# Kernel optimization log

Hardware: AMD Instinct MI355X
Metric: run time of the kernel (lower is better)

The kernel has to match this reference:

```python
import jax, jax.numpy as jnp
import numpy as np

DIMS = 256
HID = 512


def setup_inputs() -> dict:
    key = jax.random.key(0)
    ks = jax.random.split(key, 12)
    s = 0.1
    inp = {
        'x': jax.random.normal(ks[0], (64, 2048, DIMS), dtype=jnp.float32),
        'h': jnp.zeros((64, HID), jnp.float32),
        'c': jnp.zeros((64, HID), jnp.float32),
        'W_j': jax.random.normal(ks[1], (DIMS, HID), jnp.float32) * s,
        'W_i': jax.random.normal(ks[2], (DIMS, HID), jnp.float32) * s,
        'W_f': jax.random.normal(ks[3], (DIMS, HID), jnp.float32) * s,
        'W_o': jax.random.normal(ks[4], (DIMS, HID), jnp.float32) * s,
        'U_j': jax.random.normal(ks[5], (HID, HID), jnp.float32) * s,
        'U_i': jax.random.normal(ks[6], (HID, HID), jnp.float32) * s,
        'U_f': jax.random.normal(ks[7], (HID, HID), jnp.float32) * s,
        'U_o': jax.random.normal(ks[8], (HID, HID), jnp.float32) * s,
        'b_j': jnp.zeros((1, HID), jnp.float32),
        'b_i': jnp.zeros((1, HID), jnp.float32),
        'b_f': jnp.zeros((1, HID), jnp.float32),
        'b_o': jnp.zeros((1, HID), jnp.float32),
        'W_y': jax.random.normal(ks[9], (HID, DIMS), jnp.float32) * s,
        'b_y': jnp.zeros((1, DIMS), jnp.float32),
    }
    return inp


def reference(x, h, c, W_j, W_i, W_f, W_o, U_j, U_i, U_f, U_o,
              b_j, b_i, b_f, b_o, W_y, b_y):
    # Precompute input projections for all timesteps: [B,T,H] -> [T,B,H]
    xj = jnp.einsum('btd,dh->tbh', x, W_j) + b_j
    xi = jnp.einsum('btd,dh->tbh', x, W_i) + b_i
    xf = jnp.einsum('btd,dh->tbh', x, W_f) + b_f
    xo = jnp.einsum('btd,dh->tbh', x, W_o) + b_o

    def step(carry, xs):
        h, c = carry
        pj, pi, pf, po = xs
        # NOTE: module defaults -> j,i,o sigmoid; f tanh; cell activation tanh
        j = jax.nn.sigmoid(pj + h @ U_j)
        i = jax.nn.sigmoid(pi + h @ U_i)
        f = jnp.tanh(pf + h @ U_f)
        o = jax.nn.sigmoid(po + h @ U_o)
        c = f * c + i * j
        h = o * jnp.tanh(c)
        return (h, c), h

    (h_last, c_last), hs = jax.lax.scan(step, (h, c), (xj, xi, xf, xo))
    # hs: [T,B,H] -> y_hat: [B,T,dims]
    y_hat = jnp.einsum('tbh,hd->btd', hs, W_y) + b_y
    return y_hat, h_last, c_last
```

## Files before the change

kernel.cpp:

```cpp
#include <hip/hip_runtime.h>


typedef __attribute__((ext_vector_type(8))) short bf16x8;
typedef __attribute__((ext_vector_type(4))) float f32x4;

#define T_STEPS 2048
#define DIMS 256
#define HID 512

#define NPACK_U  1048576
#define NPACK_WX 524288
#define NPACK_WY 131072

#define OFF_UHI   0u
#define OFF_ULO   2097152u
#define OFF_WXHI  4194304u
#define OFF_WXLO  5242880u
#define OFF_WYHI  6291456u
#define OFF_WYLO  6553600u
#define OFF_HBUF  6815744u
#define OFF_FLAGS 7077888u

__device__ __forceinline__ unsigned short f2bf(float f) {
    unsigned u = __float_as_uint(f);
    return (unsigned short)((u + 0x7fffu + ((u >> 16) & 1u)) >> 16);
}
__device__ __forceinline__ float bf2f(unsigned short h) {
    return __uint_as_float((unsigned)h << 16);
}
__device__ __forceinline__ void split2(float f, unsigned short& hi, unsigned short& lo) {
    hi = f2bf(f);
    lo = f2bf(f - bf2f(hi));
}
__device__ __forceinline__ float sigf(float x) { return 1.0f / (1.0f + __expf(-x)); }
__device__ __forceinline__ float tanhfast(float x) { return 2.0f * sigf(2.0f * x) - 1.0f; }

__global__ void lstm_prep(const float* __restrict__ Uj, const float* __restrict__ Ui,
                          const float* __restrict__ Uf, const float* __restrict__ Uo,
                          const float* __restrict__ Wj, const float* __restrict__ Wi,
                          const float* __restrict__ Wf, const float* __restrict__ Wo,
                          const float* __restrict__ Wy,
                          unsigned short* __restrict__ Uph, unsigned short* __restrict__ Upl,
                          unsigned short* __restrict__ Wxh, unsigned short* __restrict__ Wxl,
                          unsigned short* __restrict__ Wyh, unsigned short* __restrict__ Wyl,
                          unsigned* __restrict__ flags) {
    int idx = blockIdx.x * 256 + threadIdx.x;
    if (idx < NPACK_U) {
        int j = idx & 7, l = (idx >> 3) & 63, ks = (idx >> 9) & 15, nt = (idx >> 13) & 7, s = (idx >> 16) & 15;
        int gate = nt >> 1;
        int hu = s * 32 + (nt & 1) * 16 + (l & 15);
        int k = ks * 32 + ((l >> 4) << 3) + j;
        const float* U = (gate == 0) ? Uj : (gate == 1) ? Ui : (gate == 2) ? Uf : Uo;
        unsigned short hi, lo; split2(U[k * HID + hu], hi, lo);
        Uph[idx] = hi; Upl[idx] = lo;
    } else if (idx < NPACK_U + NPACK_WX) {
        int i2 = idx - NPACK_U;
        int j = i2 & 7, l = (i2 >> 3) & 63, ks = (i2 >> 9) & 7, nt = (i2 >> 12) & 7, s = (i2 >> 15) & 15;
        int gate = nt >> 1;
        int hu = s * 32 + (nt & 1) * 16 + (l & 15);
        int k = ks * 32 + ((l >> 4) << 3) + j;
        const float* W = (gate == 0) ? Wj : (gate == 1) ? Wi : (gate == 2) ? Wf : Wo;
        unsigned short hi, lo; split2(W[k * HID + hu], hi, lo);
        Wxh[i2] = hi; Wxl[i2] = lo;
    } else if (idx < NPACK_U + NPACK_WX + NPACK_WY) {
        int i3 = idx - NPACK_U - NPACK_WX;
        int j = i3 & 7, l = (i3 >> 3) & 63, ks = (i3 >> 9) & 15, s = (i3 >> 13) & 15;
        int k = ks * 32 + ((l >> 4) << 3) + j;
        int col = s * 16 + (l & 15);
        unsigned short hi, lo; split2(Wy[k * DIMS + col], hi, lo);
        Wyh[i3] = hi; Wyl[i3] = lo;
    } else if (idx < NPACK_U + NPACK_WX + NPACK_WY + 64) {
        flags[idx - (NPACK_U + NPACK_WX + NPACK_WY)] = 0u;
    }
}

__global__ __launch_bounds__(256, 1) void lstm_scan(
    const float* __restrict__ x, const float* __restrict__ h0, const float* __restrict__ c0,
    const float* __restrict__ bj_g, const float* __restrict__ bi_g,
    const float* __restrict__ bf_g, const float* __restrict__ bo_g,
    const float* __restrict__ by_g,
    const unsigned short* __restrict__ Uph, const unsigned short* __restrict__ Upl,
    const unsigned short* __restrict__ Wxph, const unsigned short* __restrict__ Wxpl,
    const unsigned short* __restrict__ Wyph, const unsigned short* __restrict__ Wypl,
    unsigned* __restrict__ hbuf32, unsigned* __restrict__ flags,
    float* __restrict__ out)
{
    __shared__ unsigned short xsh[16][264];
    __shared__ unsigned short xsl[16][264];
    __shared__ unsigned short hsh[16][520];
    __shared__ unsigned short hsl[16][520];
    __shared__ float pre[8][16][17];
    __shared__ float yp[4][16][17];
    __shared__ float cbuf[16][32];

    const int tid = threadIdx.x;
    const int wv = tid >> 6;
    const int l = tid & 63;
    const int quad = l >> 4;
    const int lm = l & 15;
    const int g = blockIdx.x >> 4;
    const int s = blockIdx.x & 15;

    bf16x8 bUh[2][16], bUl[2][16], bWxh[2][8], bWxl[2][8], bWyh[4], bWyl[4];
    {
        const bf16x8* UH = reinterpret_cast<const bf16x8*>(Uph);
        const bf16x8* UL = reinterpret_cast<const bf16x8*>(Upl);
        const bf16x8* WH = reinterpret_cast<const bf16x8*>(Wxph);
        const bf16x8* WL = reinterpret_cast<const bf16x8*>(Wxpl);
        const bf16x8* YH = reinterpret_cast<const bf16x8*>(Wyph);
        const bf16x8* YL = reinterpret_cast<const bf16x8*>(Wypl);
        #pragma unroll
        for (int i = 0; i < 2; ++i) {
            int nt = 2 * wv + i;
            #pragma unroll
            for (int ks = 0; ks < 16; ++ks) {
                bUh[i][ks] = UH[((s * 8 + nt) * 16 + ks) * 64 + l];
                bUl[i][ks] = UL[((s * 8 + nt) * 16 + ks) * 64 + l];
            }
            #pragma unroll
            for (int ks = 0; ks < 8; ++ks) {
                bWxh[i][ks] = WH[((s * 8 + nt) * 8 + ks) * 64 + l];
                bWxl[i][ks] = WL[((s * 8 + nt) * 8 + ks) * 64 + l];
            }
        }
        #pragma unroll
        for (int q = 0; q < 4; ++q) {
            bWyh[q] = YH[(s * 16 + wv * 4 + q) * 64 + l];
            bWyl[q] = YL[(s * 16 + wv * 4 + q) * 64 + l];
        }
    }

    const int rr = tid >> 4;
    const int uu = (tid & 15) * 2;
    cbuf[rr][uu]     = c0[(size_t)(g * 16 + rr) * HID + s * 32 + uu];
    cbuf[rr][uu + 1] = c0[(size_t)(g * 16 + rr) * HID + s * 32 + uu + 1];
    float bj0 = bj_g[s * 32 + uu], bj1 = bj_g[s * 32 + uu + 1];
    float bi0 = bi_g[s * 32 + uu], bi1 = bi_g[s * 32 + uu + 1];
    float bf0 = bf_g[s * 32 + uu], bf1 = bf_g[s * 32 + uu + 1];
    float bo0 = bo_g[s * 32 + uu], bo1 = bo_g[s * 32 + uu + 1];
    const float by = by_g[s * 16 + (tid & 15)];

    const int rS = tid >> 4;
    const int cS16 = (tid & 15) * 16;
    const int cS32 = (tid & 15) * 32;
    long long budget = 1ll << 24;

    __syncthreads();

    for (int t = 0; t < T_STEPS; ++t) {
        {
            const float4* xv = reinterpret_cast<const float4*>(
                x + (size_t)(g * 16 + rS) * (T_STEPS * DIMS) + (size_t)t * DIMS + cS16);
            uint4* xdh = reinterpret_cast<uint4*>(&xsh[rS][cS16]);
            uint4* xdl = reinterpret_cast<uint4*>(&xsl[rS][cS16]);
            #pragma unroll
            for (int k = 0; k < 2; ++k) {
                float4 fa = xv[2 * k], fb = xv[2 * k + 1];
                unsigned short h0_, l0_, h1_, l1_, h2_, l2_, h3_, l3_;
                unsigned short h4_, l4_, h5_, l5_, h6_, l6_, h7_, l7_;
                split2(fa.x, h0_, l0_); split2(fa.y, h1_, l1_);
                split2(fa.z, h2_, l2_); split2(fa.w, h3_, l3_);
                split2(fb.x, h4_, l4_); split2(fb.y, h5_, l5_);
                split2(fb.z, h6_, l6_); split2(fb.w, h7_, l7_);
                uint4 uh, ul;
                uh.x = (unsigned)h0_ | ((unsigned)h1_ << 16);
                uh.y = (unsigned)h2_ | ((unsigned)h3_ << 16);
                uh.z = (unsigned)h4_ | ((unsigned)h5_ << 16);
                uh.w = (unsigned)h6_ | ((unsigned)h7_ << 16);
                ul.x = (unsigned)l0_ | ((unsigned)l1_ << 16);
                ul.y = (unsigned)l2_ | ((unsigned)l3_ << 16);
                ul.z = (unsigned)l4_ | ((unsigned)l5_ << 16);
                ul.w = (unsigned)l6_ | ((unsigned)l7_ << 16);
                xdh[k] = uh; xdl[k] = ul;
            }
        }
        __syncthreads();
        f32x4 acc0 = {0.f, 0.f, 0.f, 0.f}, acc1 = {0.f, 0.f, 0.f, 0.f};
        #pragma unroll
        for (int ks = 0; ks < 8; ++ks) {
            bf16x8 ah = *reinterpret_cast<const bf16x8*>(&xsh[lm][ks * 32 + quad * 8]);
            bf16x8 al = *reinterpret_cast<const bf16x8*>(&xsl[lm][ks * 32 + quad * 8]);
            acc0 = __builtin_amdgcn_mfma_f32_16x16x32_bf16(ah, bWxh[0][ks], acc0, 0, 0, 0);
            acc0 = __builtin_amdgcn_mfma_f32_16x16x32_bf16(al, bWxh[0][ks], acc0, 0, 0, 0);
            acc0 = __builtin_amdgcn_mfma_f32_16x16x32_bf16(ah, bWxl[0][ks], acc0, 0, 0, 0);
            acc1 = __builtin_amdgcn_mfma_f32_16x16x32_bf16(ah, bWxh[1][ks], acc1, 0, 0, 0);
            acc1 = __builtin_amdgcn_mfma_f32_16x16x32_bf16(al, bWxh[1][ks], acc1, 0, 0, 0);
            acc1 = __builtin_amdgcn_mfma_f32_16x16x32_bf16(ah, bWxl[1][ks], acc1, 0, 0, 0);
        }

        if (t > 0) {
            const unsigned target = 16u * (unsigned)t;
            while (budget > 0) {
                unsigned v = __hip_atomic_load(&flags[g], __ATOMIC_RELAXED, __HIP_MEMORY_SCOPE_AGENT);
                if (v >= target) break;
                --budget;
            }
            asm volatile("" ::: "memory");
            const unsigned base = (unsigned)(((t - 1) & 1) * 32768) + (unsigned)(g * 16 + rS) * 256
                                  + (unsigned)(tid & 15) * 16;
            const unsigned long long* sh = reinterpret_cast<const unsigned long long*>(hbuf32 + base);
            const unsigned long long* sl = reinterpret_cast<const unsigned long long*>(hbuf32 + 16384 + base);
            unsigned long long vh[8], vl[8];
            #pragma unroll
            for (int k = 0; k < 8; ++k)
                vh[k] = __hip_atomic_load(&sh[k], __ATOMIC_RELAXED, __HIP_MEMORY_SCOPE_AGENT);
            #pragma unroll
            for (int k = 0; k < 8; ++k)
                vl[k] = __hip_atomic_load(&sl[k], __ATOMIC_RELAXED, __HIP_MEMORY_SCOPE_AGENT);
            unsigned long long* dh = reinterpret_cast<unsigned long long*>(&hsh[rS][cS32]);
            unsigned long long* dl = reinterpret_cast<unsigned long long*>(&hsl[rS][cS32]);
            #pragma unroll
            for (int k = 0; k < 8; ++k) dh[k] = vh[k];
            #pragma unroll
            for (int k = 0; k < 8; ++k) dl[k] = vl[k];
        } else {
            const float4* hv = reinterpret_cast<const float4*>(
                h0 + (size_t)(g * 16 + rS) * HID + cS32);
            unsigned* hdh = reinterpret_cast<unsigned*>(&hsh[rS][cS32]);
            unsigned* hdl = reinterpret_cast<unsigned*>(&hsl[rS][cS32]);
            #pragma unroll
            for (int k = 0; k < 8; ++k) {
                float4 f = hv[k];
                unsigned short a0, b0, a1, b1, a2, b2, a3, b3;
                split2(f.x, a0, b0); split2(f.y, a1, b1);
                split2(f.z, a2, b2); split2(f.w, a3, b3);
                hdh[2 * k]     = (unsigned)a0 | ((unsigned)a1 << 16);
                hdh[2 * k + 1] = (unsigned)a2 | ((unsigned)a3 << 16);
                hdl[2 * k]     = (unsigned)b0 | ((unsigned)b1 << 16);
                hdl[2 * k + 1] = (unsigned)b2 | ((unsigned)b3 << 16);
            }
        }
        __syncthreads();

        #pragma unroll
        for (int ks = 0; ks < 16; ++ks) {
            bf16x8 ah = *reinterpret_cast<const bf16x8*>(&hsh[lm][ks * 32 + quad * 8]);
            bf16x8 al = *reinterpret_cast<const bf16x8*>(&hsl[lm][ks * 32 + quad * 8]);
            acc0 = __builtin_amdgcn_mfma_f32_16x16x32_bf16(ah, bUh[0][ks], acc0, 0, 0, 0);
            acc0 = __builtin_amdgcn_mfma_f32_16x16x32_bf16(al, bUh[0][ks], acc0, 0, 0, 0);
            acc0 = __builtin_amdgcn_mfma_f32_16x16x32_bf16(ah, bUl[0][ks], acc0, 0, 0, 0);
            acc1 = __builtin_amdgcn_mfma_f32_16x16x32_bf16(ah, bUh[1][ks], acc1, 0, 0, 0);
            acc1 = __builtin_amdgcn_mfma_f32_16x16x32_bf16(al, bUh[1][ks], acc1, 0, 0, 0);
            acc1 = __builtin_amdgcn_mfma_f32_16x16x32_bf16(ah, bUl[1][ks], acc1, 0, 0, 0);
        }
        f32x4 yacc = {0.f, 0.f, 0.f, 0.f};
        if (t > 0) {
            #pragma unroll
            for (int q = 0; q < 4; ++q) {
                bf16x8 ah = *reinterpret_cast<const bf16x8*>(&hsh[lm][(wv * 4 + q) * 32 + quad * 8]);
                bf16x8 al = *reinterpret_cast<const bf16x8*>(&hsl[lm][(wv * 4 + q) * 32 + quad * 8]);
                yacc = __builtin_amdgcn_mfma_f32_16x16x32_bf16(ah, bWyh[q], yacc, 0, 0, 0);
                yacc = __builtin_amdgcn_mfma_f32_16x16x32_bf16(al, bWyh[q], yacc, 0, 0, 0);
                yacc = __builtin_amdgcn_mfma_f32_16x16x32_bf16(ah, bWyl[q], yacc, 0, 0, 0);
            }
        }
        #pragma unroll
        for (int r = 0; r < 4; ++r) {
            pre[2 * wv][quad * 4 + r][lm]     = acc0[r];
            pre[2 * wv + 1][quad * 4 + r][lm] = acc1[r];
            yp[wv][quad * 4 + r][lm]          = yacc[r];
        }
        __syncthreads();

        {
            unsigned short hh[2], hl[2];
            #pragma unroll
            for (int d = 0; d < 2; ++d) {
                int u = uu + d;
                int nt = u >> 4, cc = u & 15;
                float pj = pre[nt][rr][cc]     + (d ? bj1 : bj0);
                float pi = pre[2 + nt][rr][cc] + (d ? bi1 : bi0);
                float pf = pre[4 + nt][rr][cc] + (d ? bf1 : bf0);
                float po = pre[6 + nt][rr][cc] + (d ? bo1 : bo0);
                float jj = sigf(pj), ii = sigf(pi), ff = tanhfast(pf), oo = sigf(po);
                float cn = ff * cbuf[rr][u] + ii * jj;
                cbuf[rr][u] = cn;
                float hn = oo * tanhfast(cn);
                split2(hn, hh[d], hl[d]);
            }
            unsigned pkh = (unsigned)hh[0] | ((unsigned)hh[1] << 16);
            unsigned pkl = (unsigned)hl[0] | ((unsigned)hl[1] << 16);
            unsigned wbase = (unsigned)((t & 1) * 32768) + (unsigned)(g * 16 + rr) * 256
                             + (unsigned)s * 16 + (unsigned)(tid & 15);
            __hip_atomic_store(hbuf32 + wbase, pkh, __ATOMIC_RELAXED, __HIP_MEMORY_SCOPE_AGENT);
            __hip_atomic_store(hbuf32 + 16384 + wbase, pkl, __ATOMIC_RELAXED, __HIP_MEMORY_SCOPE_AGENT);
        }
        asm volatile("s_waitcnt vmcnt(0)" ::: "memory");
        __syncthreads();
        if (tid == 0)
            (void)__hip_atomic_fetch_add(&flags[g], 1u, __ATOMIC_RELAXED, __HIP_MEMORY_SCOPE_AGENT);

        if (t > 0) {
            int row = tid >> 4, col = tid & 15;
            float yv = yp[0][row][col] + yp[1][row][col] + yp[2][row][col] + yp[3][row][col] + by;
            out[(size_t)(g * 16 + row) * (T_STEPS * DIMS) + (size_t)(t - 1) * DIMS + s * 16 + col] = yv;
        }
    }

    {
        const unsigned target = 16u * (unsigned)T_STEPS;
        while (budget > 0) {
            unsigned v = __hip_atomic_load(&flags[g], __ATOMIC_RELAXED, __HIP_MEMORY_SCOPE_AGENT);
            if (v >= target) break;
            --budget;
        }
        asm volatile("" ::: "memory");
        const unsigned base = (unsigned)(((T_STEPS - 1) & 1) * 32768) + (unsigned)(g * 16 + rS) * 256
                              + (unsigned)(tid & 15) * 16;
        const unsigned long long* sh = reinterpret_cast<const unsigned long long*>(hbuf32 + base);
        const unsigned long long* sl = reinterpret_cast<const unsigned long long*>(hbuf32 + 16384 + base);
        unsigned long long vh[8], vl[8];
        #pragma unroll
        for (int k = 0; k < 8; ++k)
            vh[k] = __hip_atomic_load(&sh[k], __ATOMIC_RELAXED, __HIP_MEMORY_SCOPE_AGENT);
        #pragma unroll
        for (int k = 0; k < 8; ++k)
            vl[k] = __hip_atomic_load(&sl[k], __ATOMIC_RELAXED, __HIP_MEMORY_SCOPE_AGENT);
        unsigned long long* dh = reinterpret_cast<unsigned long long*>(&hsh[rS][cS32]);
        unsigned long long* dl = reinterpret_cast<unsigned long long*>(&hsl[rS][cS32]);
        #pragma unroll
        for (int k = 0; k < 8; ++k) dh[k] = vh[k];
        #pragma unroll
        for (int k = 0; k < 8; ++k) dl[k] = vl[k];
        __syncthreads();
        f32x4 yacc = {0.f, 0.f, 0.f, 0.f};
        #pragma unroll
        for (int q = 0; q < 4; ++q) {
            bf16x8 ah = *reinterpret_cast<const bf16x8*>(&hsh[lm][(wv * 4 + q) * 32 + quad * 8]);
            bf16x8 al = *reinterpret_cast<const bf16x8*>(&hsl[lm][(wv * 4 + q) * 32 + quad * 8]);
            yacc = __builtin_amdgcn_mfma_f32_16x16x32_bf16(ah, bWyh[q], yacc, 0, 0, 0);
            yacc = __builtin_amdgcn_mfma_f32_16x16x32_bf16(al, bWyh[q], yacc, 0, 0, 0);
            yacc = __builtin_amdgcn_mfma_f32_16x16x32_bf16(ah, bWyl[q], yacc, 0, 0, 0);
        }
        #pragma unroll
        for (int r = 0; r < 4; ++r) yp[wv][quad * 4 + r][lm] = yacc[r];
        __syncthreads();
        int row = tid >> 4, col = tid & 15;
        float yv = yp[0][row][col] + yp[1][row][col] + yp[2][row][col] + yp[3][row][col] + by;
        out[(size_t)(g * 16 + row) * (T_STEPS * DIMS) + (size_t)(T_STEPS - 1) * DIMS + s * 16 + col] = yv;

        const size_t YO = (size_t)64 * T_STEPS * DIMS;
        const size_t CO = YO + (size_t)64 * HID;
        #pragma unroll
        for (int d = 0; d < 2; ++d) {
            int u = uu + d;
            out[YO + (size_t)(g * 16 + rr) * HID + s * 32 + u] =
                bf2f(hsh[rr][s * 32 + u]) + bf2f(hsl[rr][s * 32 + u]);
            out[CO + (size_t)(g * 16 + rr) * HID + s * 32 + u] = cbuf[rr][u];
        }
    }
}

extern "C" void kernel_launch(void* const* d_in, const int* in_sizes, int n_in,
                              void* d_out, int out_size, void* d_ws, size_t ws_size,
                              hipStream_t stream) {
    const float* x  = (const float*)d_in[0];
    const float* h0 = (const float*)d_in[1];
    const float* c0 = (const float*)d_in[2];
    const float* Wj = (const float*)d_in[3];
    const float* Wi = (const float*)d_in[4];
    const float* Wf = (const float*)d_in[5];
    const float* Wo = (const float*)d_in[6];
    const float* Uj = (const float*)d_in[7];
    const float* Ui = (const float*)d_in[8];
    const float* Uf = (const float*)d_in[9];
    const float* Uo = (const float*)d_in[10];
    const float* bj = (const float*)d_in[11];
    const float* bi = (const float*)d_in[12];
    const float* bf = (const float*)d_in[13];
    const float* bo = (const float*)d_in[14];
    const float* Wy = (const float*)d_in[15];
    const float* by = (const float*)d_in[16];

    char* ws = (char*)d_ws;
    unsigned short* Uph = (unsigned short*)(ws + OFF_UHI);
    unsigned short* Upl = (unsigned short*)(ws + OFF_ULO);
    unsigned short* Wxh = (unsigned short*)(ws + OFF_WXHI);
    unsigned short* Wxl = (unsigned short*)(ws + OFF_WXLO);
    unsigned short* Wyh = (unsigned short*)(ws + OFF_WYHI);
    unsigned short* Wyl = (unsigned short*)(ws + OFF_WYLO);
    unsigned* hbuf32    = (unsigned*)(ws + OFF_HBUF);
    unsigned* flags     = (unsigned*)(ws + OFF_FLAGS);
    float* out          = (float*)d_out;

    int prep_total = NPACK_U + NPACK_WX + NPACK_WY + 64;
    int prep_blocks = (prep_total + 255) / 256;
    hipLaunchKernelGGL(lstm_prep, dim3(prep_blocks), dim3(256), 0, stream,
                       Uj, Ui, Uf, Uo, Wj, Wi, Wf, Wo, Wy,
                       Uph, Upl, Wxh, Wxl, Wyh, Wyl, flags);
    hipLaunchKernelGGL(lstm_scan, dim3(64), dim3(256), 0, stream,
                       x, h0, c0, bj, bi, bf, bo, by,
                       Uph, Upl, Wxh, Wxl, Wyh, Wyl, hbuf32, flags, out);
}
```

Before: 12.66 ms.

## Prefetch x, interleave hi/lo h exchange, move Wy projection off critical path

Prefetches the next timestep's x row into registers so the global load overlaps the current step. Interleaves the hi/lo halves of the exchanged hidden state into one 64-bit word, so each producer issues a single atomic store and each consumer reads one contiguous region. Moves the previous-step output projection (Wy MFMAs) to after the flag increment, taking it off the inter-block dependency chain; this adds one extra __syncthreads per step. It also remaps the block index so the four batch groups of a hidden slice have adjacent block ids, which likely changes XCD/L2 placement of the blocks that synchronize with each other.

```diff
diff --git a/kernel.cpp b/kernel.cpp
--- a/kernel.cpp
+++ b/kernel.cpp
@@ -82,7 +82,7 @@
     const unsigned short* __restrict__ Uph, const unsigned short* __restrict__ Upl,
     const unsigned short* __restrict__ Wxph, const unsigned short* __restrict__ Wxpl,
     const unsigned short* __restrict__ Wyph, const unsigned short* __restrict__ Wypl,
-    unsigned* __restrict__ hbuf32, unsigned* __restrict__ flags,
+    unsigned long long* __restrict__ hbuf64, unsigned* __restrict__ flags,
     float* __restrict__ out)
 {
     __shared__ unsigned short xsh[16][264];
@@ -98,8 +98,8 @@
     const int l = tid & 63;
     const int quad = l >> 4;
     const int lm = l & 15;
-    const int g = blockIdx.x >> 4;
-    const int s = blockIdx.x & 15;
+    const int g = blockIdx.x & 3;
+    const int s = blockIdx.x >> 2;
 
     bf16x8 bUh[2][16], bUl[2][16], bWxh[2][8], bWxl[2][8], bWyh[4], bWyl[4];
     {
@@ -145,34 +145,54 @@
     const int cS32 = (tid & 15) * 32;
     long long budget = 1ll << 24;
 
+    float4 xr[4];
+    {
+        const float4* xv = reinterpret_cast<const float4*>(
+            x + (size_t)(g * 16 + rS) * (T_STEPS * DIMS) + cS16);
+        xr[0] = xv[0]; xr[1] = xv[1]; xr[2] = xv[2]; xr[3] = xv[3];
+    }
+
     __syncthreads();
 
     for (int t = 0; t < T_STEPS; ++t) {
         {
-            const float4* xv = reinterpret_cast<const float4*>(
-                x + (size_t)(g * 16 + rS) * (T_STEPS * DIMS) + (size_t)t * DIMS + cS16);
+            float4 f0 = xr[0], f1 = xr[1], f2 = xr[2], f3 = xr[3];
+            if (t + 1 < T_STEPS) {
+                const float4* xv = reinterpret_cast<const float4*>(
+                    x + (size_t)(g * 16 + rS) * (T_STEPS * DIMS) + (size_t)(t + 1) * DIMS + cS16);
+                xr[0] = xv[0]; xr[1] = xv[1]; xr[2] = xv[2]; xr[3] = xv[3];
+            }
             uint4* xdh = reinterpret_cast<uint4*>(&xsh[rS][cS16]);
             uint4* xdl = reinterpret_cast<uint4*>(&xsl[rS][cS16]);
-            #pragma unroll
-            for (int k = 0; k < 2; ++k) {
-                float4 fa = xv[2 * k], fb = xv[2 * k + 1];
-                unsigned short h0_, l0_, h1_, l1_, h2_, l2_, h3_, l3_;
-                unsigned short h4_, l4_, h5_, l5_, h6_, l6_, h7_, l7_;
-                split2(fa.x, h0_, l0_); split2(fa.y, h1_, l1_);
-                split2(fa.z, h2_, l2_); split2(fa.w, h3_, l3_);
-                split2(fb.x, h4_, l4_); split2(fb.y, h5_, l5_);
-                split2(fb.z, h6_, l6_); split2(fb.w, h7_, l7_);
-                uint4 uh, ul;
-                uh.x = (unsigned)h0_ | ((unsigned)h1_ << 16);
-                uh.y = (unsigned)h2_ | ((unsigned)h3_ << 16);
-                uh.z = (unsigned)h4_ | ((unsigned)h5_ << 16);
-                uh.w = (unsigned)h6_ | ((unsigned)h7_ << 16);
-                ul.x = (unsigned)l0_ | ((unsigned)l1_ << 16);
-                ul.y = (unsigned)l2_ | ((unsigned)l3_ << 16);
-                ul.z = (unsigned)l4_ | ((unsigned)l5_ << 16);
-                ul.w = (unsigned)l6_ | ((unsigned)l7_ << 16);
-                xdh[k] = uh; xdl[k] = ul;
-            }
+            unsigned short h0_, l0_, h1_, l1_, h2_, l2_, h3_, l3_;
+            unsigned short h4_, l4_, h5_, l5_, h6_, l6_, h7_, l7_;
+            uint4 uh, ul;
+            split2(f0.x, h0_, l0_); split2(f0.y, h1_, l1_);
+            split2(f0.z, h2_, l2_); split2(f0.w, h3_, l3_);
+            split2(f1.x, h4_, l4_); split2(f1.y, h5_, l5_);
+            split2(f1.z, h6_, l6_); split2(f1.w, h7_, l7_);
+            uh.x = (unsigned)h0_ | ((unsigned)h1_ << 16);
+            uh.y = (unsigned)h2_ | ((unsigned)h3_ << 16);
+            uh.z = (unsigned)h4_ | ((unsigned)h5_ << 16);
+            uh.w = (unsigned)h6_ | ((unsigned)h7_ << 16);
+            ul.x = (unsigned)l0_ | ((unsigned)l1_ << 16);
+            ul.y = (unsigned)l2_ | ((unsigned)l3_ << 16);
+            ul.z = (unsigned)l4_ | ((unsigned)l5_ << 16);
+            ul.w = (unsigned)l6_ | ((unsigned)l7_ << 16);
+            xdh[0] = uh; xdl[0] = ul;
+            split2(f2.x, h0_, l0_); split2(f2.y, h1_, l1_);
+            split2(f2.z, h2_, l2_); split2(f2.w, h3_, l3_);
+            split2(f3.x, h4_, l4_); split2(f3.y, h5_, l5_);
+            split2(f3.z, h6_, l6_); split2(f3.w, h7_, l7_);
+            uh.x = (unsigned)h0_ | ((unsigned)h1_ << 16);
+            uh.y = (unsigned)h2_ | ((unsigned)h3_ << 16);
+            uh.z = (unsigned)h4_ | ((unsigned)h5_ << 16);
+            uh.w = (unsigned)h6_ | ((unsigned)h7_ << 16);
+            ul.x = (unsigned)l0_ | ((unsigned)l1_ << 16);
+            ul.y = (unsigned)l2_ | ((unsigned)l3_ << 16);
+            ul.z = (unsigned)l4_ | ((unsigned)l5_ << 16);
+            ul.w = (unsigned)l6_ | ((unsigned)l7_ << 16);
+            xdh[1] = uh; xdl[1] = ul;
         }
         __syncthreads();
         f32x4 acc0 = {0.f, 0.f, 0.f, 0.f}, acc1 = {0.f, 0.f, 0.f, 0.f};
@@ -196,23 +216,21 @@
                 --budget;
             }
             asm volatile("" ::: "memory");
-            const unsigned base = (unsigned)(((t - 1) & 1) * 32768) + (unsigned)(g * 16 + rS) * 256
-                                  + (unsigned)(tid & 15) * 16;
-            const unsigned long long* sh = reinterpret_cast<const unsigned long long*>(hbuf32 + base);
-            const unsigned long long* sl = reinterpret_cast<const unsigned long long*>(hbuf32 + 16384 + base);
-            unsigned long long vh[8], vl[8];
-            #pragma unroll
-            for (int k = 0; k < 8; ++k)
-                vh[k] = __hip_atomic_load(&sh[k], __ATOMIC_RELAXED, __HIP_MEMORY_SCOPE_AGENT);
-            #pragma unroll
-            for (int k = 0; k < 8; ++k)
-                vl[k] = __hip_atomic_load(&sl[k], __ATOMIC_RELAXED, __HIP_MEMORY_SCOPE_AGENT);
+            const unsigned long long* src = hbuf64 + (unsigned)(((t - 1) & 1) * 16384)
+                                            + (unsigned)(g * 16 + rS) * 256 + (unsigned)(tid & 15) * 16;
+            unsigned long long v64[16];
+            #pragma unroll
+            for (int k = 0; k < 16; ++k)
+                v64[k] = __hip_atomic_load(&src[k], __ATOMIC_RELAXED, __HIP_MEMORY_SCOPE_AGENT);
             unsigned long long* dh = reinterpret_cast<unsigned long long*>(&hsh[rS][cS32]);
             unsigned long long* dl = reinterpret_cast<unsigned long long*>(&hsl[rS][cS32]);
             #pragma unroll
-            for (int k = 0; k < 8; ++k) dh[k] = vh[k];
-            #pragma unroll
-            for (int k = 0; k < 8; ++k) dl[k] = vl[k];
+            for (int m = 0; m < 8; ++m) {
+                dh[m] = (unsigned long long)(unsigned)v64[2 * m]
+                        | ((unsigned long long)(unsigned)v64[2 * m + 1] << 32);
+                dl[m] = (unsigned long long)(unsigned)(v64[2 * m] >> 32)
+                        | ((unsigned long long)(unsigned)(v64[2 * m + 1] >> 32) << 32);
+            }
         } else {
             const float4* hv = reinterpret_cast<const float4*>(
                 h0 + (size_t)(g * 16 + rS) * HID + cS32);
@@ -243,22 +261,10 @@
             acc1 = __builtin_amdgcn_mfma_f32_16x16x32_bf16(al, bUh[1][ks], acc1, 0, 0, 0);
             acc1 = __builtin_amdgcn_mfma_f32_16x16x32_bf16(ah, bUl[1][ks], acc1, 0, 0, 0);
         }
-        f32x4 yacc = {0.f, 0.f, 0.f, 0.f};
-        if (t > 0) {
-            #pragma unroll
-            for (int q = 0; q < 4; ++q) {
-                bf16x8 ah = *reinterpret_cast<const bf16x8*>(&hsh[lm][(wv * 4 + q) * 32 + quad * 8]);
-                bf16x8 al = *reinterpret_cast<const bf16x8*>(&hsl[lm][(wv * 4 + q) * 32 + quad * 8]);
-                yacc = __builtin_amdgcn_mfma_f32_16x16x32_bf16(ah, bWyh[q], yacc, 0, 0, 0);
-                yacc = __builtin_amdgcn_mfma_f32_16x16x32_bf16(al, bWyh[q], yacc, 0, 0, 0);
-                yacc = __builtin_amdgcn_mfma_f32_16x16x32_bf16(ah, bWyl[q], yacc, 0, 0, 0);
-            }
-        }
         #pragma unroll
         for (int r = 0; r < 4; ++r) {
             pre[2 * wv][quad * 4 + r][lm]     = acc0[r];
             pre[2 * wv + 1][quad * 4 + r][lm] = acc1[r];
-            yp[wv][quad * 4 + r][lm]          = yacc[r];
         }
         __syncthreads();
 
@@ -280,10 +286,10 @@
             }
             unsigned pkh = (unsigned)hh[0] | ((unsigned)hh[1] << 16);
             unsigned pkl = (unsigned)hl[0] | ((unsigned)hl[1] << 16);
-            unsigned wbase = (unsigned)((t & 1) * 32768) + (unsigned)(g * 16 + rr) * 256
+            unsigned long long hv64 = (unsigned long long)pkh | ((unsigned long long)pkl << 32);
+            unsigned wbase = (unsigned)((t & 1) * 16384) + (unsigned)(g * 16 + rr) * 256
                              + (unsigned)s * 16 + (unsigned)(tid & 15);
-            __hip_atomic_store(hbuf32 + wbase, pkh, __ATOMIC_RELAXED, __HIP_MEMORY_SCOPE_AGENT);
-            __hip_atomic_store(hbuf32 + 16384 + wbase, pkl, __ATOMIC_RELAXED, __HIP_MEMORY_SCOPE_AGENT);
+            __hip_atomic_store(hbuf64 + wbase, hv64, __ATOMIC_RELAXED, __HIP_MEMORY_SCOPE_AGENT);
         }
         asm volatile("s_waitcnt vmcnt(0)" ::: "memory");
         __syncthreads();
@@ -291,6 +297,18 @@
             (void)__hip_atomic_fetch_add(&flags[g], 1u, __ATOMIC_RELAXED, __HIP_MEMORY_SCOPE_AGENT);
 
         if (t > 0) {
+            f32x4 yacc = {0.f, 0.f, 0.f, 0.f};
+            #pragma unroll
+            for (int q = 0; q < 4; ++q) {
+                bf16x8 ah = *reinterpret_cast<const bf16x8*>(&hsh[lm][(wv * 4 + q) * 32 + quad * 8]);
+                bf16x8 al = *reinterpret_cast<const bf16x8*>(&hsl[lm][(wv * 4 + q) * 32 + quad * 8]);
+                yacc = __builtin_amdgcn_mfma_f32_16x16x32_bf16(ah, bWyh[q], yacc, 0, 0, 0);
+                yacc = __builtin_amdgcn_mfma_f32_16x16x32_bf16(al, bWyh[q], yacc, 0, 0, 0);
+                yacc = __builtin_amdgcn_mfma_f32_16x16x32_bf16(ah, bWyl[q], yacc, 0, 0, 0);
+            }
+            #pragma unroll
+            for (int r = 0; r < 4; ++r) yp[wv][quad * 4 + r][lm] = yacc[r];
+            __syncthreads();
             int row = tid >> 4, col = tid & 15;
             float yv = yp[0][row][col] + yp[1][row][col] + yp[2][row][col] + yp[3][row][col] + by;
             out[(size_t)(g * 16 + row) * (T_STEPS * DIMS) + (size_t)(t - 1) * DIMS + s * 16 + col] = yv;
@@ -305,23 +323,21 @@
             --budget;
         }
         asm volatile("" ::: "memory");
-        const unsigned base = (unsigned)(((T_STEPS - 1) & 1) * 32768) + (unsigned)(g * 16 + rS) * 256
-                              + (unsigned)(tid & 15) * 16;
-        const unsigned long long* sh = reinterpret_cast<const unsigned long long*>(hbuf32 + base);
-        const unsigned long long* sl = reinterpret_cast<const unsigned long long*>(hbuf32 + 16384 + base);
-        unsigned long long vh[8], vl[8];
-        #pragma unroll
-        for (int k = 0; k < 8; ++k)
-            vh[k] = __hip_atomic_load(&sh[k], __ATOMIC_RELAXED, __HIP_MEMORY_SCOPE_AGENT);
-        #pragma unroll
-        for (int k = 0; k < 8; ++k)
-            vl[k] = __hip_atomic_load(&sl[k], __ATOMIC_RELAXED, __HIP_MEMORY_SCOPE_AGENT);
+        const unsigned long long* src = hbuf64 + (unsigned)(((T_STEPS - 1) & 1) * 16384)
+                                        + (unsigned)(g * 16 + rS) * 256 + (unsigned)(tid & 15) * 16;
+        unsigned long long v64[16];
+        #pragma unroll
+        for (int k = 0; k < 16; ++k)
+            v64[k] = __hip_atomic_load(&src[k], __ATOMIC_RELAXED, __HIP_MEMORY_SCOPE_AGENT);
         unsigned long long* dh = reinterpret_cast<unsigned long long*>(&hsh[rS][cS32]);
         unsigned long long* dl = reinterpret_cast<unsigned long long*>(&hsl[rS][cS32]);
         #pragma unroll
-        for (int k = 0; k < 8; ++k) dh[k] = vh[k];
-        #pragma unroll
-        for (int k = 0; k < 8; ++k) dl[k] = vl[k];
+        for (int m = 0; m < 8; ++m) {
+            dh[m] = (unsigned long long)(unsigned)v64[2 * m]
+                    | ((unsigned long long)(unsigned)v64[2 * m + 1] << 32);
+            dl[m] = (unsigned long long)(unsigned)(v64[2 * m] >> 32)
+                    | ((unsigned long long)(unsigned)(v64[2 * m + 1] >> 32) << 32);
+        }
         __syncthreads();
         f32x4 yacc = {0.f, 0.f, 0.f, 0.f};
         #pragma unroll
@@ -379,7 +395,7 @@
     unsigned short* Wxl = (unsigned short*)(ws + OFF_WXLO);
     unsigned short* Wyh = (unsigned short*)(ws + OFF_WYHI);
     unsigned short* Wyl = (unsigned short*)(ws + OFF_WYLO);
-    unsigned* hbuf32    = (unsigned*)(ws + OFF_HBUF);
+    unsigned long long* hbuf64 = (unsigned long long*)(ws + OFF_HBUF);
     unsigned* flags     = (unsigned*)(ws + OFF_FLAGS);
     float* out          = (float*)d_out;
 
@@ -390,5 +406,5 @@
                        Uph, Upl, Wxh, Wxl, Wyh, Wyl, flags);
     hipLaunchKernelGGL(lstm_scan, dim3(64), dim3(256), 0, stream,
                        x, h0, c0, bj, bi, bf, bo, by,
-                       Uph, Upl, Wxh, Wxl, Wyh, Wyl, hbuf32, flags, out);
-}
+                       Uph, Upl, Wxh, Wxl, Wyh, Wyl, hbuf64, flags, out);
+}
```

Result: slower. 14.44 ms (+14.1%).

## Prefetch next-step x into registers and move output projection off the critical path

Applied to the files above, without the earlier changes.

Loads the next timestep's x slice into registers during the current step, right after the flag spin, so the global load latency overlaps with the recurrent matmul instead of stalling the start of each step. The W_y output projection MFMAs are moved to after the h stores to the global exchange buffer, and a sched_barrier keeps them there. The aim is to publish h to other blocks sooner, shortening the cross-block dependency chain. The cost is extra register pressure from holding four float4 values across the loop.

```diff
diff --git a/kernel.cpp b/kernel.cpp
--- a/kernel.cpp
+++ b/kernel.cpp
@@ -145,34 +145,49 @@
     const int cS32 = (tid & 15) * 32;
     long long budget = 1ll << 24;
 
+    float4 xr[4];
+    {
+        const float4* xv = reinterpret_cast<const float4*>(
+            x + (size_t)(g * 16 + rS) * (T_STEPS * DIMS) + cS16);
+        xr[0] = xv[0]; xr[1] = xv[1]; xr[2] = xv[2]; xr[3] = xv[3];
+    }
+
     __syncthreads();
 
     for (int t = 0; t < T_STEPS; ++t) {
         {
-            const float4* xv = reinterpret_cast<const float4*>(
-                x + (size_t)(g * 16 + rS) * (T_STEPS * DIMS) + (size_t)t * DIMS + cS16);
+            float4 f0 = xr[0], f1 = xr[1], f2 = xr[2], f3 = xr[3];
             uint4* xdh = reinterpret_cast<uint4*>(&xsh[rS][cS16]);
             uint4* xdl = reinterpret_cast<uint4*>(&xsl[rS][cS16]);
-            #pragma unroll
-            for (int k = 0; k < 2; ++k) {
-                float4 fa = xv[2 * k], fb = xv[2 * k + 1];
-                unsigned short h0_, l0_, h1_, l1_, h2_, l2_, h3_, l3_;
-                unsigned short h4_, l4_, h5_, l5_, h6_, l6_, h7_, l7_;
-                split2(fa.x, h0_, l0_); split2(fa.y, h1_, l1_);
-                split2(fa.z, h2_, l2_); split2(fa.w, h3_, l3_);
-                split2(fb.x, h4_, l4_); split2(fb.y, h5_, l5_);
-                split2(fb.z, h6_, l6_); split2(fb.w, h7_, l7_);
-                uint4 uh, ul;
-                uh.x = (unsigned)h0_ | ((unsigned)h1_ << 16);
-                uh.y = (unsigned)h2_ | ((unsigned)h3_ << 16);
-                uh.z = (unsigned)h4_ | ((unsigned)h5_ << 16);
-                uh.w = (unsigned)h6_ | ((unsigned)h7_ << 16);
-                ul.x = (unsigned)l0_ | ((unsigned)l1_ << 16);
-                ul.y = (unsigned)l2_ | ((unsigned)l3_ << 16);
-                ul.z = (unsigned)l4_ | ((unsigned)l5_ << 16);
-                ul.w = (unsigned)l6_ | ((unsigned)l7_ << 16);
-                xdh[k] = uh; xdl[k] = ul;
-            }
+            unsigned short h0_, l0_, h1_, l1_, h2_, l2_, h3_, l3_;
+            unsigned short h4_, l4_, h5_, l5_, h6_, l6_, h7_, l7_;
+            uint4 uh, ul;
+            split2(f0.x, h0_, l0_); split2(f0.y, h1_, l1_);
+            split2(f0.z, h2_, l2_); split2(f0.w, h3_, l3_);
+            split2(f1.x, h4_, l4_); split2(f1.y, h5_, l5_);
+            split2(f1.z, h6_, l6_); split2(f1.w, h7_, l7_);
+            uh.x = (unsigned)h0_ | ((unsigned)h1_ << 16);
+            uh.y = (unsigned)h2_ | ((unsigned)h3_ << 16);
+            uh.z = (unsigned)h4_ | ((unsigned)h5_ << 16);
+            uh.w = (unsigned)h6_ | ((unsigned)h7_ << 16);
+            ul.x = (unsigned)l0_ | ((unsigned)l1_ << 16);
+            ul.y = (unsigned)l2_ | ((unsigned)l3_ << 16);
+            ul.z = (unsigned)l4_ | ((unsigned)l5_ << 16);
+            ul.w = (unsigned)l6_ | ((unsigned)l7_ << 16);
+            xdh[0] = uh; xdl[0] = ul;
+            split2(f2.x, h0_, l0_); split2(f2.y, h1_, l1_);
+            split2(f2.z, h2_, l2_); split2(f2.w, h3_, l3_);
+            split2(f3.x, h4_, l4_); split2(f3.y, h5_, l5_);
+            split2(f3.z, h6_, l6_); split2(f3.w, h7_, l7_);
+            uh.x = (unsigned)h0_ | ((unsigned)h1_ << 16);
+            uh.y = (unsigned)h2_ | ((unsigned)h3_ << 16);
+            uh.z = (unsigned)h4_ | ((unsigned)h5_ << 16);
+            uh.w = (unsigned)h6_ | ((unsigned)h7_ << 16);
+            ul.x = (unsigned)l0_ | ((unsigned)l1_ << 16);
+            ul.y = (unsigned)l2_ | ((unsigned)l3_ << 16);
+            ul.z = (unsigned)l4_ | ((unsigned)l5_ << 16);
+            ul.w = (unsigned)l6_ | ((unsigned)l7_ << 16);
+            xdh[1] = uh; xdl[1] = ul;
         }
         __syncthreads();
         f32x4 acc0 = {0.f, 0.f, 0.f, 0.f}, acc1 = {0.f, 0.f, 0.f, 0.f};
@@ -196,6 +211,11 @@
                 --budget;
             }
             asm volatile("" ::: "memory");
+            if (t + 1 < T_STEPS) {
+                const float4* xv = reinterpret_cast<const float4*>(
+                    x + (size_t)(g * 16 + rS) * (T_STEPS * DIMS) + (size_t)(t + 1) * DIMS + cS16);
+                xr[0] = xv[0]; xr[1] = xv[1]; xr[2] = xv[2]; xr[3] = xv[3];
+            }
             const unsigned base = (unsigned)(((t - 1) & 1) * 32768) + (unsigned)(g * 16 + rS) * 256
                                   + (unsigned)(tid & 15) * 16;
             const unsigned long long* sh = reinterpret_cast<const unsigned long long*>(hbuf32 + base);
@@ -214,6 +234,9 @@
             #pragma unroll
             for (int k = 0; k < 8; ++k) dl[k] = vl[k];
         } else {
+            const float4* xv = reinterpret_cast<const float4*>(
+                x + (size_t)(g * 16 + rS) * (T_STEPS * DIMS) + (size_t)1 * DIMS + cS16);
+            xr[0] = xv[0]; xr[1] = xv[1]; xr[2] = xv[2]; xr[3] = xv[3];
             const float4* hv = reinterpret_cast<const float4*>(
                 h0 + (size_t)(g * 16 + rS) * HID + cS32);
             unsigned* hdh = reinterpret_cast<unsigned*>(&hsh[rS][cS32]);
@@ -243,22 +266,10 @@
             acc1 = __builtin_amdgcn_mfma_f32_16x16x32_bf16(al, bUh[1][ks], acc1, 0, 0, 0);
             acc1 = __builtin_amdgcn_mfma_f32_16x16x32_bf16(ah, bUl[1][ks], acc1, 0, 0, 0);
         }
-        f32x4 yacc = {0.f, 0.f, 0.f, 0.f};
-        if (t > 0) {
-            #pragma unroll
-            for (int q = 0; q < 4; ++q) {
-                bf16x8 ah = *reinterpret_cast<const bf16x8*>(&hsh[lm][(wv * 4 + q) * 32 + quad * 8]);
-                bf16x8 al = *reinterpret_cast<const bf16x8*>(&hsl[lm][(wv * 4 + q) * 32 + quad * 8]);
-                yacc = __builtin_amdgcn_mfma_f32_16x16x32_bf16(ah, bWyh[q], yacc, 0, 0, 0);
-                yacc = __builtin_amdgcn_mfma_f32_16x16x32_bf16(al, bWyh[q], yacc, 0, 0, 0);
-                yacc = __builtin_amdgcn_mfma_f32_16x16x32_bf16(ah, bWyl[q], yacc, 0, 0, 0);
-            }
-        }
         #pragma unroll
         for (int r = 0; r < 4; ++r) {
             pre[2 * wv][quad * 4 + r][lm]     = acc0[r];
             pre[2 * wv + 1][quad * 4 + r][lm] = acc1[r];
-            yp[wv][quad * 4 + r][lm]          = yacc[r];
         }
         __syncthreads();
 
@@ -284,6 +295,21 @@
                              + (unsigned)s * 16 + (unsigned)(tid & 15);
             __hip_atomic_store(hbuf32 + wbase, pkh, __ATOMIC_RELAXED, __HIP_MEMORY_SCOPE_AGENT);
             __hip_atomic_store(hbuf32 + 16384 + wbase, pkl, __ATOMIC_RELAXED, __HIP_MEMORY_SCOPE_AGENT);
+        }
+        __builtin_amdgcn_sched_barrier(0);
+
+        f32x4 yacc = {0.f, 0.f, 0.f, 0.f};
+        if (t > 0) {
+            #pragma unroll
+            for (int q = 0; q < 4; ++q) {
+                bf16x8 ah = *reinterpret_cast<const bf16x8*>(&hsh[lm][(wv * 4 + q) * 32 + quad * 8]);
+                bf16x8 al = *reinterpret_cast<const bf16x8*>(&hsl[lm][(wv * 4 + q) * 32 + quad * 8]);
+                yacc = __builtin_amdgcn_mfma_f32_16x16x32_bf16(ah, bWyh[q], yacc, 0, 0, 0);
+                yacc = __builtin_amdgcn_mfma_f32_16x16x32_bf16(al, bWyh[q], yacc, 0, 0, 0);
+                yacc = __builtin_amdgcn_mfma_f32_16x16x32_bf16(ah, bWyl[q], yacc, 0, 0, 0);
+            }
+            #pragma unroll
+            for (int r = 0; r < 4; ++r) yp[wv][quad * 4 + r][lm] = yacc[r];
         }
         asm volatile("s_waitcnt vmcnt(0)" ::: "memory");
         __syncthreads();
```

After: 13.15 ms. +3.9%, slower.
